# Optimization experiments

Hardware: AMD Instinct MI355X
Metric: run time of the kernel (lower is better)

Reference implementation:

```python
import jax, jax.numpy as jnp
import numpy as np

DN = ('NCHW', 'OIHW', 'NCHW')

def conv(x, w, b=None, stride=1, pad=0):
    y = jax.lax.conv_general_dilated(x, w, (stride, stride), [(pad, pad), (pad, pad)],
                                     dimension_numbers=DN)
    return y if b is None else y + b[None, :, None, None]

def conv_t(x, w, b, stride=2, pad=1):
    # PyTorch ConvTranspose2d: w is (in, out, kh, kw); equivalent to an
    # input-dilated conv with spatially flipped, in/out-swapped kernel.
    k = w.shape[2]
    w2 = jnp.flip(w, (2, 3)).transpose(1, 0, 2, 3)
    p = k - 1 - pad
    y = jax.lax.conv_general_dilated(x, w2, (1, 1), [(p, p), (p, p)],
                                     lhs_dilation=(stride, stride), dimension_numbers=DN)
    return y + b[None, :, None, None]

def res_block(x, wa, wb):
    h = conv(jax.nn.relu(x), wa, None, 1, 1)   # 3x3, no bias
    h = conv(jax.nn.relu(h), wb, None, 1, 0)   # 1x1, no bias
    return x + h

def vq(x, codebook):
    B, C, H, W = x.shape
    xf = x.transpose(0, 2, 3, 1).reshape(-1, C)                      # (N, D)
    d = ((xf * xf).sum(-1, keepdims=True)
         - 2.0 * xf @ codebook.T
         + (codebook * codebook).sum(-1)[None, :])
    idx = jnp.argmin(d, axis=1)                                      # (N,)
    q = jnp.take(codebook, idx, axis=0)                              # gather (N, D)
    return q.reshape(B, H, W, C).transpose(0, 3, 1, 2)

def setup_inputs() -> dict:
    key = jax.random.key(0)
    ks = jax.random.split(key, 16)
    r = lambda i, shape: jax.random.normal(ks[i], shape, jnp.float32) * 0.05
    K, D = 512, 64
    return {
        'x': jax.random.normal(ks[0], (32, 1, 256, 256), jnp.float32),
        'w_e1': r(1, (32, 1, 4, 4)),   'b_e1': jnp.zeros((32,), jnp.float32),
        'w_e2': r(2, (64, 32, 4, 4)),  'b_e2': jnp.zeros((64,), jnp.float32),
        'w_er1a': r(3, (32, 64, 3, 3)), 'w_er1b': r(4, (64, 32, 1, 1)),
        'w_er2a': r(5, (32, 64, 3, 3)), 'w_er2b': r(6, (64, 32, 1, 1)),
        'w_pre': r(7, (D, 64, 1, 1)),  'b_pre': jnp.zeros((D,), jnp.float32),
        'codebook': jax.random.uniform(ks[8], (K, D), jnp.float32, -1.0 / K, 1.0 / K),
        'w_d1': r(9, (64, D, 3, 3)),   'b_d1': jnp.zeros((64,), jnp.float32),
        'w_dr1a': r(10, (32, 64, 3, 3)), 'w_dr1b': r(11, (64, 32, 1, 1)),
        'w_dr2a': r(12, (32, 64, 3, 3)), 'w_dr2b': r(13, (64, 32, 1, 1)),
        'w_t1': r(14, (64, 32, 4, 4)), 'b_t1': jnp.zeros((32,), jnp.float32),
        'w_t2': r(15, (32, 1, 4, 4)),  'b_t2': jnp.zeros((1,), jnp.float32),
    }

def reference(x, w_e1, b_e1, w_e2, b_e2, w_er1a, w_er1b, w_er2a, w_er2b,
              w_pre, b_pre, codebook, w_d1, b_d1, w_dr1a, w_dr1b,
              w_dr2a, w_dr2b, w_t1, b_t1, w_t2, b_t2):
    # Encoder
    h = jax.nn.relu(conv(x, w_e1, b_e1, 2, 1))     # (B,32,128,128)
    h = conv(h, w_e2, b_e2, 2, 1)                  # (B,64,64,64)
    h = res_block(h, w_er1a, w_er1b)
    h = res_block(h, w_er2a, w_er2b)
    # pre-VQ 1x1 conv
    h = conv(h, w_pre, b_pre, 1, 0)                # (B,64,64,64)
    # Vector quantization
    q = vq(h, codebook)
    # Decoder
    d = conv(q, w_d1, b_d1, 1, 1)
    d = res_block(d, w_dr1a, w_dr1b)
    d = res_block(d, w_dr2a, w_dr2b)
    d = jax.nn.relu(conv_t(d, w_t1, b_t1))         # (B,32,128,128)
    d = conv_t(d, w_t2, b_t2)                      # (B,1,256,256)
    return d
```

## Files before the change

kernel.cpp:

```cpp
#include <hip/hip_runtime.h>
#include <hip/hip_bf16.h>


__device__ __forceinline__ float rp_elem(const float* __restrict__ src,
                                         int i, int COUT, int CIN, int KK)
{
    const int co = i % COUT;
    const int t  = i / COUT;
    const int kk = t % KK;
    const int ci = t / KK;
    return src[(co * CIN + ci) * KK + kk];
}

__global__ __launch_bounds__(256) void repack_all(
    const float* __restrict__ e1,  const float* __restrict__ e2,
    const float* __restrict__ er1a, const float* __restrict__ er1b,
    const float* __restrict__ er2a, const float* __restrict__ er2b,
    const float* __restrict__ pre, const float* __restrict__ d1,
    const float* __restrict__ dr1a, const float* __restrict__ dr1b,
    const float* __restrict__ dr2a, const float* __restrict__ dr2b,
    const float* __restrict__ t1, const float* __restrict__ cb,
    float* __restrict__ WR)
{
    const int idx = blockIdx.x * 256 + threadIdx.x;
    if (idx >= 221696) return;
    float v;
    if      (idx < 512)    v = rp_elem(e1,   idx,          32,  1, 16);
    else if (idx < 33280)  v = rp_elem(e2,   idx - 512,    64, 32, 16);
    else if (idx < 51712)  v = rp_elem(er1a, idx - 33280,  32, 64,  9);
    else if (idx < 53760)  v = rp_elem(er1b, idx - 51712,  64, 32,  1);
    else if (idx < 72192)  v = rp_elem(er2a, idx - 53760,  32, 64,  9);
    else if (idx < 74240)  v = rp_elem(er2b, idx - 72192,  64, 32,  1);
    else if (idx < 78336)  v = rp_elem(pre,  idx - 74240,  64, 64,  1);
    else if (idx < 115200) v = rp_elem(d1,   idx - 78336,  64, 64,  9);
    else if (idx < 133632) v = rp_elem(dr1a, idx - 115200, 32, 64,  9);
    else if (idx < 135680) v = rp_elem(dr1b, idx - 133632, 64, 32,  1);
    else if (idx < 154112) v = rp_elem(dr2a, idx - 135680, 32, 64,  9);
    else if (idx < 156160) v = rp_elem(dr2b, idx - 154112, 64, 32,  1);
    else if (idx < 188928) {
        const int i  = idx - 156160;
        const int co = i & 31;
        const int q  = (i >> 5) & 3;
        const int k2 = (i >> 7) & 127;
        const int pr = i >> 14;
        const int pc = q >> 1, tb = q & 1;
        const int ci = k2 >> 1, ta = k2 & 1;
        const int kh = (1 - pr) + 2 * ta, kw = (1 - pc) + 2 * tb;
        v = t1[((ci * 32 + co) * 4 + kh) * 4 + kw];
    } else {
        const int i = idx - 188928;
        const int code = i & 511;
        const int dim  = i >> 9;
        v = cb[code * 64 + dim];
    }
    WR[idx] = v;
}

__global__ __launch_bounds__(256) void vq_prep_ee(
    const float* __restrict__ cb, float* __restrict__ ee)
{
    const int k = blockIdx.x * 256 + threadIdx.x;
    const float* __restrict__ cp = cb + (size_t)k * 64;
    float s = 0.0f;
#pragma unroll
    for (int i = 0; i < 64; i++) s = fmaf(cp[i], cp[i], s);
    ee[k] = s;
}

template<int CTOT, int CPB, int CIN, int K, int S, int PAD,
         bool RELU_IN, bool HAS_BIAS, bool RESID, bool RELU_OUT>
__global__ __launch_bounds__(256) void conv_gemm(
    const float* __restrict__ in, const float* __restrict__ wr,
    const float* __restrict__ bias, const float* __restrict__ resid,
    float* __restrict__ out,
    int H, int W, int OH, int OW)
{
    constexpr int KK  = K * K;
    constexpr int CIC = (K == 1) ? 8 : 1;
    constexpr int TS  = (K == 4) ? 2 : 1;
    constexpr int KC  = CIC * KK / TS;
    constexpr int NCH = (CIN * TS) / CIC;
    constexpr int NT  = 256;
    constexpr int CPTHD = CPB / 4;
    __shared__ __align__(16) float As[2][KC * NT];

    const int tid = threadIdx.x;
    const int tpx = tid & 63;
    const int tco = __builtin_amdgcn_readfirstlane(tid >> 6);
    const int co0 = blockIdx.y * CPB + tco * CPTHD;

    const int ohow = OH * OW;
    const int n_st = blockIdx.x * NT + tid;
    const int b_st = n_st / ohow;
    const int hw_s = n_st % ohow;
    const int ih0 = (hw_s / OW) * S - PAD;
    const int iw0 = (hw_s % OW) * S - PAD;
    const float* __restrict__ inb = in + (size_t)b_st * CIN * H * W;

    float acc[CPTHD][4];
#pragma unroll
    for (int c = 0; c < CPTHD; c++) {
        const float bz = HAS_BIAS ? bias[co0 + c] : 0.0f;
#pragma unroll
        for (int q = 0; q < 4; q++) acc[c][q] = bz;
    }

    float pf[KC];
    auto stage_load = [&](int ch) {
#pragma unroll
        for (int t = 0; t < KC; t++) {
            int ci, kh, kw;
            if constexpr (K == 1) {
                ci = ch * 8 + t; kh = 0; kw = 0;
            } else if constexpr (K == 3) {
                ci = ch; kh = t / 3; kw = t % 3;
            } else {
                ci = ch >> 1;
                const int kk = ((ch & 1) << 3) + t;
                kh = kk >> 2; kw = kk & 3;
            }
            const int ih = ih0 + kh, iw = iw0 + kw;
            float v = 0.0f;
            if (ih >= 0 && ih < H && iw >= 0 && iw < W)
                v = inb[(size_t)ci * H * W + ih * W + iw];
            if (RELU_IN) v = fmaxf(v, 0.0f);
            pf[t] = v;
        }
    };

    stage_load(0);
#pragma unroll
    for (int t = 0; t < KC; t++) As[0][t * NT + tid] = pf[t];
    __syncthreads();

#pragma unroll 2
    for (int c = 0; c < NCH; c++) {
        const int cur = c & 1;
        if (c + 1 < NCH) stage_load(c + 1);

#pragma unroll
        for (int t = 0; t < KC; t++) {
            const float4 a4 = *(const float4*)(As[cur] + t * NT + tpx * 4);
            const float* __restrict__ wk =
                wr + (size_t)(c * KC + t) * CTOT + co0;
#pragma unroll
            for (int cc = 0; cc < CPTHD; cc++) {
                const float w = wk[cc];
                acc[cc][0] = fmaf(a4.x, w, acc[cc][0]);
                acc[cc][1] = fmaf(a4.y, w, acc[cc][1]);
                acc[cc][2] = fmaf(a4.z, w, acc[cc][2]);
                acc[cc][3] = fmaf(a4.w, w, acc[cc][3]);
            }
        }

        if (c + 1 < NCH) {
#pragma unroll
            for (int t = 0; t < KC; t++) As[1 - cur][t * NT + tid] = pf[t];
        }
        __syncthreads();
    }

    const int n_c  = blockIdx.x * NT + tpx * 4;
    const int b_c  = n_c / ohow;
    const int hw_c = n_c % ohow;
    float* __restrict__ op = out + (size_t)b_c * CTOT * ohow + hw_c;
    const float* __restrict__ rp =
        RESID ? (resid + (size_t)b_c * CTOT * ohow + hw_c) : nullptr;
#pragma unroll
    for (int c = 0; c < CPTHD; c++) {
        const size_t off = (size_t)(co0 + c) * ohow;
        float4 r = make_float4(acc[c][0], acc[c][1], acc[c][2], acc[c][3]);
        if (RESID) {
            const float4 rv = *(const float4*)(rp + off);
            r.x += rv.x; r.y += rv.y; r.z += rv.z; r.w += rv.w;
        }
        if (RELU_OUT) {
            r.x = fmaxf(r.x, 0.f); r.y = fmaxf(r.y, 0.f);
            r.z = fmaxf(r.z, 0.f); r.w = fmaxf(r.w, 0.f);
        }
        *(float4*)(op + off) = r;
    }
}

__global__ __launch_bounds__(512, 4) void res_tile(
    const float* __restrict__ in, const float* __restrict__ wr1,
    const float* __restrict__ wr2, float* __restrict__ out)
{
    __shared__ __align__(16) float S[13824];

    const int tid = threadIdx.x;
    const int p   = tid & 127;
    const int cog = __builtin_amdgcn_readfirstlane(tid >> 7);
    const int a   = p >> 5;
    const int c0  = (p & 31) * 2;

    const int n0   = blockIdx.x * 256;
    const int b    = n0 >> 12;
    const int row0 = (n0 & 4095) >> 6;
    const float* __restrict__ inb = in + (size_t)b * 64 * 4096;

    float4 pf4[7];
    auto stage_issue = [&](int half) {
#pragma unroll
        for (int m = 0; m < 7; m++) {
            const int f4 = m * 512 + tid;
            float4 v = make_float4(0.f, 0.f, 0.f, 0.f);
            if (f4 < 3456) {
                const int ci  = f4 / 108;
                const int rem = f4 - ci * 108;
                const int r6  = rem / 18;
                const int c4  = rem - r6 * 18;
                const int ih  = row0 + r6 - 1;
                if (ih >= 0 && ih < 64 && c4 >= 1 && c4 <= 16)
                    v = *(const float4*)(inb + (size_t)(half * 32 + ci) * 4096
                                         + ih * 64 + (c4 * 4 - 4));
            }
            pf4[m] = v;
        }
    };
    auto stage_commit = [&]() {
#pragma unroll
        for (int m = 0; m < 7; m++) {
            const int f4 = m * 512 + tid;
            if (f4 < 3456) {
                float4 v = pf4[m];
                v.x = fmaxf(v.x, 0.f); v.y = fmaxf(v.y, 0.f);
                v.z = fmaxf(v.z, 0.f); v.w = fmaxf(v.w, 0.f);
                *(float4*)(S + f4 * 4) = v;
            }
        }
    };

    const int co1 = cog * 8;
    float acc1[8][2];
#pragma unroll
    for (int c = 0; c < 8; c++) { acc1[c][0] = 0.0f; acc1[c][1] = 0.0f; }

    auto conv1_half = [&](int h) {
#pragma unroll 2
        for (int c = 0; c < 32; c++) {
            const float* __restrict__ wb =
                wr1 + (size_t)((h * 32 + c) * 9) * 32 + co1;
#pragma unroll
            for (int kh = 0; kh < 3; kh++) {
                const float* __restrict__ tp =
                    S + c * 432 + (a + kh) * 72 + 4 + c0;
                const float2 L = *(const float2*)(tp - 2);
                const float2 M = *(const float2*)(tp);
                const float2 R = *(const float2*)(tp + 2);
                const float xm = L.y;
                const float x0 = M.x;
                const float x1 = M.y;
                const float x2 = R.x;
                const float* __restrict__ wk = wb + (size_t)(kh * 3) * 32;
#pragma unroll
                for (int cc = 0; cc < 8; cc++) {
                    const float w = wk[cc];
                    acc1[cc][0] = fmaf(xm, w, acc1[cc][0]);
                    acc1[cc][1] = fmaf(x0, w, acc1[cc][1]);
                }
#pragma unroll
                for (int cc = 0; cc < 8; cc++) {
                    const float w = wk[32 + cc];
                    acc1[cc][0] = fmaf(x0, w, acc1[cc][0]);
                    acc1[cc][1] = fmaf(x1, w, acc1[cc][1]);
                }
#pragma unroll
                for (int cc = 0; cc < 8; cc++) {
                    const float w = wk[64 + cc];
                    acc1[cc][0] = fmaf(x1, w, acc1[cc][0]);
                    acc1[cc][1] = fmaf(x2, w, acc1[cc][1]);
                }
            }
        }
    };

    stage_issue(0);
    stage_commit();
    __syncthreads();
    stage_issue(1);
    conv1_half(0);
    __syncthreads();
    stage_commit();
    __syncthreads();
    conv1_half(1);
    __syncthreads();

#pragma unroll
    for (int cc = 0; cc < 8; cc++)
        *(float2*)(S + (co1 + cc) * 256 + p * 2) =
            make_float2(acc1[cc][0], acc1[cc][1]);
    __syncthreads();

    const int co2 = cog * 16;
    float acc2[16][2];
#pragma unroll
    for (int c = 0; c < 16; c++) { acc2[c][0] = 0.0f; acc2[c][1] = 0.0f; }

#pragma unroll 4
    for (int k = 0; k < 32; k++) {
        float2 m2 = *(const float2*)(S + k * 256 + p * 2);
        m2.x = fmaxf(m2.x, 0.f);
        m2.y = fmaxf(m2.y, 0.f);
        const float* __restrict__ wk = wr2 + (size_t)k * 64 + co2;
#pragma unroll
        for (int cc = 0; cc < 16; cc++) {
            const float w = wk[cc];
            acc2[cc][0] = fmaf(m2.x, w, acc2[cc][0]);
            acc2[cc][1] = fmaf(m2.y, w, acc2[cc][1]);
        }
    }

    const int hw = (n0 & 4095) + p * 2;
    const float* __restrict__ rp = inb + hw;
    float* __restrict__ op = out + (size_t)b * 64 * 4096 + hw;
#pragma unroll
    for (int cc = 0; cc < 16; cc++) {
        const size_t off = (size_t)(co2 + cc) * 4096;
        const float2 rv = *(const float2*)(rp + off);
        *(float2*)(op + off) =
            make_float2(acc2[cc][0] + rv.x, acc2[cc][1] + rv.y);
    }
}

__global__ __launch_bounds__(256) void convt_gemm2(
    const float* __restrict__ in, const float* __restrict__ wr,
    const float* __restrict__ bias, float* __restrict__ out)
{
    constexpr int NT = 256;
    __shared__ __align__(16) float As[2][12 * NT];

    const int tid = threadIdx.x;
    const int tpx = tid & 63;
    const int tco = __builtin_amdgcn_readfirstlane(tid >> 6);
    const int pr = blockIdx.y & 1;
    const int cg = blockIdx.y >> 1;
    const int co0 = cg * 16 + tco * 4;

    const int n_st = blockIdx.x * NT + tid;
    const int b = n_st >> 12;
    const int i_st = (n_st & 4095) >> 6;
    const int j_st = n_st & 63;
    const float* __restrict__ inb = in + (size_t)b * 64 * 4096;

    float acc[4][4][2];
#pragma unroll
    for (int c = 0; c < 4; c++) {
        const float bz = bias[co0 + c];
#pragma unroll
        for (int p = 0; p < 4; p++) {
            acc[c][p][0] = bz;
            acc[c][p][1] = bz;
        }
    }

    const float* __restrict__ wpr = wr + (size_t)pr * 128 * 4 * 32;

    float pf[12];
    auto stage_load = [&](int ch) {
#pragma unroll
        for (int t = 0; t < 4; t++) {
            const int k2 = ch * 4 + t;
            const int ci = k2 >> 1;
            const int ta = k2 & 1;
            const int ih = i_st + pr - ta;
            const bool rok = (ih >= 0) && (ih < 64);
            const float* __restrict__ row = inb + (size_t)ci * 4096 + ih * 64;
#pragma unroll
            for (int m = 0; m < 3; m++) {
                const int iw = j_st + m - 1;
                float v = 0.0f;
                if (rok && iw >= 0 && iw < 64) v = row[iw];
                pf[t * 3 + m] = v;
            }
        }
    };

    stage_load(0);
#pragma unroll
    for (int t = 0; t < 12; t++) As[0][t * NT + tid] = pf[t];
    __syncthreads();

#pragma unroll 2
    for (int ch = 0; ch < 32; ch++) {
        const int cur = ch & 1;
        if (ch + 1 < 32) stage_load(ch + 1);

#pragma unroll
        for (int t = 0; t < 4; t++) {
            float4 a[3];
#pragma unroll
            for (int m = 0; m < 3; m++)
                a[m] = *(const float4*)(As[cur] + (t * 3 + m) * NT + tpx * 4);
            const float* __restrict__ wk =
                wpr + (size_t)(ch * 4 + t) * 4 * 32 + co0;
#pragma unroll
            for (int tb = 0; tb < 2; tb++) {
#pragma unroll
                for (int pc = 0; pc < 2; pc++) {
                    const int q = pc * 2 + tb;
                    const int m = pc - tb + 1;
                    const float* __restrict__ wt = wk + q * 32;
                    const float vx = a[m].x, vy = a[m].y,
                                vz = a[m].z, vw = a[m].w;
#pragma unroll
                    for (int c = 0; c < 4; c++) {
                        const float w = wt[c];
                        acc[c][0][pc] = fmaf(vx, w, acc[c][0][pc]);
                        acc[c][1][pc] = fmaf(vy, w, acc[c][1][pc]);
                        acc[c][2][pc] = fmaf(vz, w, acc[c][2][pc]);
                        acc[c][3][pc] = fmaf(vw, w, acc[c][3][pc]);
                    }
                }
            }
        }

        if (ch + 1 < 32) {
#pragma unroll
            for (int t = 0; t < 12; t++) As[1 - cur][t * NT + tid] = pf[t];
        }
        __syncthreads();
    }

    const int n_c = blockIdx.x * NT + tpx * 4;
    const int i_c = (n_c & 4095) >> 6;
    const int j_c = n_c & 63;
    const int oh = 2 * i_c + pr;
    float* __restrict__ ob =
        out + (size_t)b * 32 * 16384 + (size_t)oh * 128 + 2 * j_c;
#pragma unroll
    for (int c = 0; c < 4; c++) {
        float* __restrict__ o = ob + (size_t)(co0 + c) * 16384;
        const float4 v0 = make_float4(
            fmaxf(acc[c][0][0], 0.f), fmaxf(acc[c][0][1], 0.f),
            fmaxf(acc[c][1][0], 0.f), fmaxf(acc[c][1][1], 0.f));
        const float4 v1 = make_float4(
            fmaxf(acc[c][2][0], 0.f), fmaxf(acc[c][2][1], 0.f),
            fmaxf(acc[c][3][0], 0.f), fmaxf(acc[c][3][1], 0.f));
        *(float4*)o = v0;
        *(float4*)(o + 4) = v1;
    }
}

__global__ __launch_bounds__(256) void convt2_quad(
    const float* __restrict__ in, const float* __restrict__ w,
    const float* __restrict__ bias, float* __restrict__ out, int B)
{
    const int IH = 128, IW = 128, CIN = 32, OW = 256;
    const int j = threadIdx.x & 127;
    const int i = (blockIdx.x << 1) + (threadIdx.x >> 7);
    const int b = blockIdx.y;

    const float* __restrict__ inb = in + (size_t)b * CIN * IH * IW;
    const float bz = bias[0];
    float a00 = bz, a01 = bz, a10 = bz, a11 = bz;

    const bool okm = (i > 0);
    const bool okp = (i < IH - 1);
    const bool olm = (j > 0);
    const bool olp = (j < IW - 1);

#pragma unroll 4
    for (int ci = 0; ci < CIN; ci++) {
        const float* __restrict__ p = inb + ((size_t)ci * IH + i) * IW + j;
        const float* __restrict__ wp = w + ci * 16;
        const float vmm = (okm && olm) ? p[-IW - 1] : 0.f;
        const float vm0 = okm ? p[-IW] : 0.f;
        const float vmp = (okm && olp) ? p[-IW + 1] : 0.f;
        const float v0m = olm ? p[-1] : 0.f;
        const float v00 = p[0];
        const float v0p = olp ? p[1] : 0.f;
        const float vpm = (okp && olm) ? p[IW - 1] : 0.f;
        const float vp0 = okp ? p[IW] : 0.f;
        const float vpp = (okp && olp) ? p[IW + 1] : 0.f;
        a00 = fmaf(v00, wp[1 * 4 + 1], a00);
        a00 = fmaf(v0m, wp[1 * 4 + 3], a00);
        a00 = fmaf(vm0, wp[3 * 4 + 1], a00);
        a00 = fmaf(vmm, wp[3 * 4 + 3], a00);
        a01 = fmaf(v0p, wp[1 * 4 + 0], a01);
        a01 = fmaf(v00, wp[1 * 4 + 2], a01);
        a01 = fmaf(vmp, wp[3 * 4 + 0], a01);
        a01 = fmaf(vm0, wp[3 * 4 + 2], a01);
        a10 = fmaf(vp0, wp[0 * 4 + 1], a10);
        a10 = fmaf(vpm, wp[0 * 4 + 3], a10);
        a10 = fmaf(v00, wp[2 * 4 + 1], a10);
        a10 = fmaf(v0m, wp[2 * 4 + 3], a10);
        a11 = fmaf(vpp, wp[0 * 4 + 0], a11);
        a11 = fmaf(vp0, wp[0 * 4 + 2], a11);
        a11 = fmaf(v0p, wp[2 * 4 + 0], a11);
        a11 = fmaf(v00, wp[2 * 4 + 2], a11);
    }

    float* __restrict__ outb = out + (size_t)b * 256 * 256;
    ((float2*)(outb + (size_t)(2 * i) * OW))[j] = make_float2(a00, a01);
    ((float2*)(outb + (size_t)(2 * i + 1) * OW))[j] = make_float2(a10, a11);
}

__global__ __launch_bounds__(256) void vq_gemm(
    const float* __restrict__ h,
    const float* __restrict__ cb,
    const float* __restrict__ cbT,
    const float* __restrict__ ee,
    float* __restrict__ q)
{
    __shared__ __align__(16) float As[64 * 128];
    __shared__ float xx_sh[128];
    __shared__ float pd[4 * 128];
    __shared__ int   pk[4 * 128];
    __shared__ int   bidx_sh[128];

    const int tid = threadIdx.x;
    const int tpx = tid & 63;
    const int w = __builtin_amdgcn_readfirstlane(tid >> 6);
    const int n0 = blockIdx.x * 128;
    const int b  = n0 >> 12;
    const int hw0 = n0 & 4095;

    const float* __restrict__ hb = h + (size_t)b * 64 * 4096 + hw0;
#pragma unroll
    for (int m = 0; m < 32; m++) {
        const int idx = m * 256 + tid;
        const int k = idx >> 7, p = idx & 127;
        As[idx] = hb[(size_t)k * 4096 + p];
    }
    __syncthreads();

    if (tid < 128) {
        float s = 0.0f;
#pragma unroll
        for (int i = 0; i < 64; i++) {
            const float v = As[i * 128 + tid];
            s = fmaf(v, v, s);
        }
        xx_sh[tid] = s;
    }
    __syncthreads();

    const float xx0 = xx_sh[tpx * 2];
    const float xx1 = xx_sh[tpx * 2 + 1];
    const int cwave = w * 128;

    float best0 = 3.402823466e+38f, best1 = 3.402823466e+38f;
    int bk0 = 0, bk1 = 0;

#pragma unroll 1
    for (int ch = 0; ch < 16; ch++) {
        const int cbase = cwave + ch * 8;
        float acc[8][2];
#pragma unroll
        for (int c = 0; c < 8; c++) { acc[c][0] = 0.0f; acc[c][1] = 0.0f; }

#pragma unroll 8
        for (int k = 0; k < 64; k++) {
            const float2 a2 = *(const float2*)(As + k * 128 + tpx * 2);
            const float* __restrict__ wk = cbT + (size_t)k * 512 + cbase;
#pragma unroll
            for (int c = 0; c < 8; c++) {
                const float wv = wk[c];
                acc[c][0] = fmaf(a2.x, wv, acc[c][0]);
                acc[c][1] = fmaf(a2.y, wv, acc[c][1]);
            }
        }
        const float* __restrict__ eep = ee + cbase;
#pragma unroll
        for (int c = 0; c < 8; c++) {
            const float eec = eep[c];
            const float d0 = xx0 - 2.0f * acc[c][0] + eec;
            const float d1 = xx1 - 2.0f * acc[c][1] + eec;
            if (d0 < best0) { best0 = d0; bk0 = cbase + c; }
            if (d1 < best1) { best1 = d1; bk1 = cbase + c; }
        }
    }

    pd[w * 128 + tpx * 2]     = best0;
    pd[w * 128 + tpx * 2 + 1] = best1;
    pk[w * 128 + tpx * 2]     = bk0;
    pk[w * 128 + tpx * 2 + 1] = bk1;
    __syncthreads();

    if (tid < 128) {
        float bd = pd[tid]; int bk = pk[tid];
#pragma unroll
        for (int ww = 1; ww < 4; ww++) {
            const float od = pd[ww * 128 + tid];
            if (od < bd) { bd = od; bk = pk[ww * 128 + tid]; }
        }
        bidx_sh[tid] = bk;
    }
    __syncthreads();

    {
        const int p  = tid & 127;
        const int d0 = (tid >> 7) * 32;
        const int bk = bidx_sh[p];
        const float4* __restrict__ cp4 = (const float4*)(cb + (size_t)bk * 64 + d0);
        float* __restrict__ qb = q + ((size_t)b * 64 + d0) * 4096 + hw0 + p;
#pragma unroll
        for (int i = 0; i < 8; i++) {
            const float4 v = cp4[i];
            qb[(size_t)(4 * i + 0) * 4096] = v.x;
            qb[(size_t)(4 * i + 1) * 4096] = v.y;
            qb[(size_t)(4 * i + 2) * 4096] = v.z;
            qb[(size_t)(4 * i + 3) * 4096] = v.w;
        }
    }
}

extern "C" void kernel_launch(void* const* d_in, const int* in_sizes, int n_in,
                              void* d_out, int out_size, void* d_ws, size_t ws_size,
                              hipStream_t stream) {
    const float* x      = (const float*)d_in[0];
    const float* w_e1   = (const float*)d_in[1];
    const float* b_e1   = (const float*)d_in[2];
    const float* w_e2   = (const float*)d_in[3];
    const float* b_e2   = (const float*)d_in[4];
    const float* w_er1a = (const float*)d_in[5];
    const float* w_er1b = (const float*)d_in[6];
    const float* w_er2a = (const float*)d_in[7];
    const float* w_er2b = (const float*)d_in[8];
    const float* w_pre  = (const float*)d_in[9];
    const float* b_pre  = (const float*)d_in[10];
    const float* cbk    = (const float*)d_in[11];
    const float* w_d1   = (const float*)d_in[12];
    const float* b_d1   = (const float*)d_in[13];
    const float* w_dr1a = (const float*)d_in[14];
    const float* w_dr1b = (const float*)d_in[15];
    const float* w_dr2a = (const float*)d_in[16];
    const float* w_dr2b = (const float*)d_in[17];
    const float* w_t1   = (const float*)d_in[18];
    const float* b_t1   = (const float*)d_in[19];
    const float* w_t2   = (const float*)d_in[20];
    const float* b_t2   = (const float*)d_in[21];
    float* out = (float*)d_out;

    float* A  = (float*)d_ws;
    float* Bb = A  + 16777216;
    float* C  = Bb + 8388608;
    float* D  = C  + 4194304;
    float* WR = D  + 8388608;
    float* EE = WR + 221696;

    float* r_e1  = WR;
    float* r_e2  = WR + 512;
    float* r_er1a = WR + 33280;
    float* r_er1b = WR + 51712;
    float* r_er2a = WR + 53760;
    float* r_er2b = WR + 72192;
    float* r_pre = WR + 74240;
    float* r_d1  = WR + 78336;
    float* r_dr1a = WR + 115200;
    float* r_dr1b = WR + 133632;
    float* r_dr2a = WR + 135680;
    float* r_dr2b = WR + 154112;
    float* r_t1  = WR + 156160;
    float* r_cbT = WR + 188928;

    const dim3 blk(256);
    const dim3 blk512(512);

    repack_all<<<dim3(866), blk, 0, stream>>>(
        w_e1, w_e2, w_er1a, w_er1b, w_er2a, w_er2b, w_pre, w_d1,
        w_dr1a, w_dr1b, w_dr2a, w_dr2b, w_t1, cbk, WR);
    vq_prep_ee<<<dim3(2), blk, 0, stream>>>(cbk, EE);

    conv_gemm<32, 32, 1, 4, 2, 1, false, true, false, true>
        <<<dim3(2048, 1), blk, 0, stream>>>(x, r_e1, b_e1, nullptr, A,
                                            256, 256, 128, 128);
    conv_gemm<64, 16, 32, 4, 2, 1, false, true, false, false>
        <<<dim3(512, 4), blk, 0, stream>>>(A, r_e2, b_e2, nullptr, Bb,
                                           128, 128, 64, 64);
    res_tile<<<dim3(512), blk512, 0, stream>>>(Bb, r_er1a, r_er1b, A);
    res_tile<<<dim3(512), blk512, 0, stream>>>(A, r_er2a, r_er2b, Bb);
    conv_gemm<64, 16, 64, 1, 1, 0, false, true, false, false>
        <<<dim3(512, 4), blk, 0, stream>>>(Bb, r_pre, b_pre, nullptr, D,
                                           64, 64, 64, 64);
    vq_gemm<<<dim3(1024), blk, 0, stream>>>(D, cbk, r_cbT, EE, Bb);
    conv_gemm<64, 16, 64, 3, 1, 1, false, true, false, false>
        <<<dim3(512, 4), blk, 0, stream>>>(Bb, r_d1, b_d1, nullptr, D,
                                           64, 64, 64, 64);
    res_tile<<<dim3(512), blk512, 0, stream>>>(D, r_dr1a, r_dr1b, A);
    res_tile<<<dim3(512), blk512, 0, stream>>>(A, r_dr2a, r_dr2b, D);
    convt_gemm2<<<dim3(512, 4), blk, 0, stream>>>(D, r_t1, b_t1, A);
    convt2_quad<<<dim3(64, 32), blk, 0, stream>>>(A, w_t2, b_t2, out, 32);
}
```

Measured before the change: 1.039 ms.

## Replace generic conv_gemm with halo-tiled direct conv kernels for e2 and d1

```diff
diff --git a/kernel.cpp b/kernel.cpp
--- a/kernel.cpp
+++ b/kernel.cpp
@@ -323,6 +323,229 @@
     }
 }
 
+__global__ __launch_bounds__(512, 4) void conv3_tile(
+    const float* __restrict__ in, const float* __restrict__ wr,
+    const float* __restrict__ bias, float* __restrict__ out)
+{
+    __shared__ __align__(16) float S[13824];
+
+    const int tid = threadIdx.x;
+    const int p   = tid & 127;
+    const int cog = __builtin_amdgcn_readfirstlane(tid >> 7);
+    const int a   = p >> 5;
+    const int c0  = (p & 31) * 2;
+
+    const int n0   = blockIdx.x * 256;
+    const int b    = n0 >> 12;
+    const int row0 = (n0 & 4095) >> 6;
+    const float* __restrict__ inb = in + (size_t)b * 64 * 4096;
+
+    float4 pf4[7];
+    auto stage_issue = [&](int half) {
+#pragma unroll
+        for (int m = 0; m < 7; m++) {
+            const int f4 = m * 512 + tid;
+            float4 v = make_float4(0.f, 0.f, 0.f, 0.f);
+            if (f4 < 3456) {
+                const int ci  = f4 / 108;
+                const int rem = f4 - ci * 108;
+                const int r6  = rem / 18;
+                const int c4  = rem - r6 * 18;
+                const int ih  = row0 + r6 - 1;
+                if (ih >= 0 && ih < 64 && c4 >= 1 && c4 <= 16)
+                    v = *(const float4*)(inb + (size_t)(half * 32 + ci) * 4096
+                                         + ih * 64 + (c4 * 4 - 4));
+            }
+            pf4[m] = v;
+        }
+    };
+    auto stage_commit = [&]() {
+#pragma unroll
+        for (int m = 0; m < 7; m++) {
+            const int f4 = m * 512 + tid;
+            if (f4 < 3456) *(float4*)(S + f4 * 4) = pf4[m];
+        }
+    };
+
+    const int co1 = cog * 16;
+    float acc[16][2];
+#pragma unroll
+    for (int cc = 0; cc < 16; cc++) {
+        const float bz = bias[co1 + cc];
+        acc[cc][0] = bz; acc[cc][1] = bz;
+    }
+
+    auto conv_half = [&](int h) {
+#pragma unroll 2
+        for (int c = 0; c < 32; c++) {
+            const float* __restrict__ wb =
+                wr + (size_t)((h * 32 + c) * 9) * 64 + co1;
+#pragma unroll
+            for (int kh = 0; kh < 3; kh++) {
+                const float* __restrict__ tp =
+                    S + c * 432 + (a + kh) * 72 + 4 + c0;
+                const float2 L = *(const float2*)(tp - 2);
+                const float2 M = *(const float2*)(tp);
+                const float2 R = *(const float2*)(tp + 2);
+                const float xm = L.y;
+                const float x0 = M.x;
+                const float x1 = M.y;
+                const float x2 = R.x;
+                const float* __restrict__ wk = wb + (size_t)(kh * 3) * 64;
+#pragma unroll
+                for (int cc = 0; cc < 16; cc++) {
+                    const float w = wk[cc];
+                    acc[cc][0] = fmaf(xm, w, acc[cc][0]);
+                    acc[cc][1] = fmaf(x0, w, acc[cc][1]);
+                }
+#pragma unroll
+                for (int cc = 0; cc < 16; cc++) {
+                    const float w = wk[64 + cc];
+                    acc[cc][0] = fmaf(x0, w, acc[cc][0]);
+                    acc[cc][1] = fmaf(x1, w, acc[cc][1]);
+                }
+#pragma unroll
+                for (int cc = 0; cc < 16; cc++) {
+                    const float w = wk[128 + cc];
+                    acc[cc][0] = fmaf(x1, w, acc[cc][0]);
+                    acc[cc][1] = fmaf(x2, w, acc[cc][1]);
+                }
+            }
+        }
+    };
+
+    stage_issue(0);
+    stage_commit();
+    __syncthreads();
+    stage_issue(1);
+    conv_half(0);
+    __syncthreads();
+    stage_commit();
+    __syncthreads();
+    conv_half(1);
+
+    const int hw = (n0 & 4095) + p * 2;
+    float* __restrict__ op = out + (size_t)b * 64 * 4096 + hw;
+#pragma unroll
+    for (int cc = 0; cc < 16; cc++)
+        *(float2*)(op + (size_t)(co1 + cc) * 4096) =
+            make_float2(acc[cc][0], acc[cc][1]);
+}
+
+__global__ __launch_bounds__(512, 4) void conv4s2_tile(
+    const float* __restrict__ in, const float* __restrict__ wr,
+    const float* __restrict__ bias, float* __restrict__ out)
+{
+    __shared__ __align__(16) float S[13056];
+
+    const int tid = threadIdx.x;
+    const int p   = tid & 63;
+    const int cog = __builtin_amdgcn_readfirstlane(tid >> 6);
+    const int a   = p >> 5;
+    const int c0  = (p & 31) * 2;
+
+    const int n0   = blockIdx.x * 128;
+    const int b    = n0 >> 12;
+    const int row0 = (n0 & 4095) >> 6;
+    const float* __restrict__ inb = in + (size_t)b * 32 * 16384;
+
+    float4 pf4[7];
+    auto stage_issue = [&](int half) {
+#pragma unroll
+        for (int m = 0; m < 7; m++) {
+            const int f4 = m * 512 + tid;
+            float4 v = make_float4(0.f, 0.f, 0.f, 0.f);
+            if (f4 < 3264) {
+                const int ci  = f4 / 204;
+                const int rem = f4 - ci * 204;
+                const int r6  = rem / 34;
+                const int s   = rem - r6 * 34;
+                const int ih  = 2 * row0 - 1 + r6;
+                if (ih >= 0 && ih < 128 && s >= 1 && s <= 32)
+                    v = *(const float4*)(inb + (size_t)(half * 16 + ci) * 16384
+                                         + ih * 128 + (s - 1) * 4);
+            }
+            pf4[m] = v;
+        }
+    };
+    auto stage_commit = [&]() {
+#pragma unroll
+        for (int m = 0; m < 7; m++) {
+            const int f4 = m * 512 + tid;
+            if (f4 < 3264) *(float4*)(S + f4 * 4) = pf4[m];
+        }
+    };
+
+    const int co1 = cog * 8;
+    float acc[8][2];
+#pragma unroll
+    for (int cc = 0; cc < 8; cc++) {
+        const float bz = bias[co1 + cc];
+        acc[cc][0] = bz; acc[cc][1] = bz;
+    }
+
+    auto conv_half = [&](int h) {
+#pragma unroll 2
+        for (int c = 0; c < 16; c++) {
+            const float* __restrict__ wb =
+                wr + (size_t)((h * 16 + c) * 16) * 64 + co1;
+#pragma unroll
+            for (int kh = 0; kh < 4; kh++) {
+                const float* __restrict__ tp =
+                    S + c * 816 + (2 * a + kh) * 136 + 2 * c0 + 2;
+                const float2 E0 = *(const float2*)(tp);
+                const float2 E1 = *(const float2*)(tp + 2);
+                const float2 E2 = *(const float2*)(tp + 4);
+                const float2 E3 = *(const float2*)(tp + 6);
+                const float x0 = E0.y, x1 = E1.x, x2 = E1.y;
+                const float x3 = E2.x, x4 = E2.y, x5 = E3.x;
+                const float* __restrict__ wk = wb + (size_t)(kh * 4) * 64;
+#pragma unroll
+                for (int cc = 0; cc < 8; cc++) {
+                    const float w = wk[cc];
+                    acc[cc][0] = fmaf(x0, w, acc[cc][0]);
+                    acc[cc][1] = fmaf(x2, w, acc[cc][1]);
+                }
+#pragma unroll
+                for (int cc = 0; cc < 8; cc++) {
+                    const float w = wk[64 + cc];
+                    acc[cc][0] = fmaf(x1, w, acc[cc][0]);
+                    acc[cc][1] = fmaf(x3, w, acc[cc][1]);
+                }
+#pragma unroll
+                for (int cc = 0; cc < 8; cc++) {
+                    const float w = wk[128 + cc];
+                    acc[cc][0] = fmaf(x2, w, acc[cc][0]);
+                    acc[cc][1] = fmaf(x4, w, acc[cc][1]);
+                }
+#pragma unroll
+                for (int cc = 0; cc < 8; cc++) {
+                    const float w = wk[192 + cc];
+                    acc[cc][0] = fmaf(x3, w, acc[cc][0]);
+                    acc[cc][1] = fmaf(x5, w, acc[cc][1]);
+                }
+            }
+        }
+    };
+
+    stage_issue(0);
+    stage_commit();
+    __syncthreads();
+    stage_issue(1);
+    conv_half(0);
+    __syncthreads();
+    stage_commit();
+    __syncthreads();
+    conv_half(1);
+
+    const int hw = (n0 & 4095) + p * 2;
+    float* __restrict__ op = out + (size_t)b * 64 * 4096 + hw;
+#pragma unroll
+    for (int cc = 0; cc < 8; cc++)
+        *(float2*)(op + (size_t)(co1 + cc) * 4096) =
+            make_float2(acc[cc][0], acc[cc][1]);
+}
+
 __global__ __launch_bounds__(256) void convt_gemm2(
     const float* __restrict__ in, const float* __restrict__ wr,
     const float* __restrict__ bias, float* __restrict__ out)
@@ -666,18 +889,14 @@
     conv_gemm<32, 32, 1, 4, 2, 1, false, true, false, true>
         <<<dim3(2048, 1), blk, 0, stream>>>(x, r_e1, b_e1, nullptr, A,
                                             256, 256, 128, 128);
-    conv_gemm<64, 16, 32, 4, 2, 1, false, true, false, false>
-        <<<dim3(512, 4), blk, 0, stream>>>(A, r_e2, b_e2, nullptr, Bb,
-                                           128, 128, 64, 64);
+    conv4s2_tile<<<dim3(1024), blk512, 0, stream>>>(A, r_e2, b_e2, Bb);
     res_tile<<<dim3(512), blk512, 0, stream>>>(Bb, r_er1a, r_er1b, A);
     res_tile<<<dim3(512), blk512, 0, stream>>>(A, r_er2a, r_er2b, Bb);
     conv_gemm<64, 16, 64, 1, 1, 0, false, true, false, false>
         <<<dim3(512, 4), blk, 0, stream>>>(Bb, r_pre, b_pre, nullptr, D,
                                            64, 64, 64, 64);
     vq_gemm<<<dim3(1024), blk, 0, stream>>>(D, cbk, r_cbT, EE, Bb);
-    conv_gemm<64, 16, 64, 3, 1, 1, false, true, false, false>
-        <<<dim3(512, 4), blk, 0, stream>>>(Bb, r_d1, b_d1, nullptr, D,
-                                           64, 64, 64, 64);
+    conv3_tile<<<dim3(512), blk512, 0, stream>>>(Bb, r_d1, b_d1, D);
     res_tile<<<dim3(512), blk512, 0, stream>>>(D, r_dr1a, r_dr1b, A);
     res_tile<<<dim3(512), blk512, 0, stream>>>(A, r_dr2a, r_dr2b, D);
     convt_gemm2<<<dim3(512, 4), blk, 0, stream>>>(D, r_t1, b_t1, A);
```

New measurement: 909.3 us. -12.5%, faster.
